# Performance work log

Hardware: AMD Instinct MI355X
Metric: run time of the kernel (lower is better)

## Reference

```python
import jax, jax.numpy as jnp
import numpy as np

N, D, M = 50000, 6, 32  # particles, state_dim, num_measurements
MD = 3                  # measurement dim (rho, alpha, epsilon)
_LOG2PI = jnp.log(2.0 * jnp.pi)


def h(x):
    # Radar measurement of a single state: uses position = x[:3]
    px, py, pz = x[0], x[1], x[2]
    rho = jnp.sqrt(px * px + py * py + pz * pz)
    return jnp.stack([rho, jnp.arctan2(py, px), jnp.arcsin(pz / rho)])


def setup_inputs() -> dict:
    key = jax.random.key(0)
    k1, k2, k3, k4 = jax.random.split(key, 4)
    scale = jnp.array([1000.0, 1000.0, 1000.0, 10.0, 10.0, 10.0], dtype=jnp.float32)
    offset = jnp.array([5000.0, 5000.0, 5000.0, 0.0, 0.0, 0.0], dtype=jnp.float32)
    means = jax.random.normal(k1, (N, D), dtype=jnp.float32) * scale + offset
    covs = jax.random.normal(k2, (N, D, D), dtype=jnp.float32)  # only used for zeros_like shape
    weights = jax.random.uniform(k3, (N,), dtype=jnp.float32)
    noise_std = jnp.array([1.0, jnp.deg2rad(0.5), jnp.deg2rad(0.5)], dtype=jnp.float32)
    measurements = jax.vmap(h)(means[:M]) + jax.random.normal(k4, (M, MD), dtype=jnp.float32) * noise_std
    measurements_mask = jnp.ones((M,), dtype=bool)
    R = jnp.diag(noise_std ** 2)  # measurement_system.covariance
    return {"means": means, "covs": covs, "weights": weights,
            "measurements": measurements, "measurements_mask": measurements_mask, "R": R}


def reference(means, covs, weights, measurements, measurements_mask, R):
    n, d = means.shape
    m = measurements.shape[0]
    md = measurements.shape[1]

    # Silverman-style bandwidth and localized empirical covariance (shared across particles)
    bandwidth = (4.0 / (n * (d + 2))) ** (2.0 / (d + 4))
    Xc = means - jnp.mean(means, axis=0)
    emp = (Xc.T @ Xc) / (n - 1)  # jnp.cov(means.T), ddof=1
    idx = jnp.arange(d)
    dist = jnp.abs(idx[:, None] - idx[None, :]).astype(means.dtype)
    rho_loc = jnp.exp(-dist ** 2 / (2.0 * 3.0 ** 2))  # L = 3.0
    P = bandwidth * (emp * rho_loc)  # [d, d] mixture covariance

    # Per-particle autodiff Jacobian of the measurement function (as in update_point)
    H = jax.vmap(jax.jacfwd(h))(means)                     # [N, md, d]
    S = jnp.einsum('nij,jk,nlk->nil', H, P, H) + R          # [N, md, md] innovation cov
    Sinv = jnp.linalg.inv(S)
    K = jnp.einsum('ij,nkj,nkl->nil', P, H, Sinv)           # [N, d, md] Kalman gain
    I = jnp.eye(d, dtype=means.dtype)
    KH = jnp.einsum('nik,nkj->nij', K, H)
    covs_post = jnp.einsum('nij,jk->nik', I - KH, P)        # [N, d, d]

    # Updated points per (measurement, particle)
    hx = jax.vmap(h)(means)                                 # [N, md]
    innov = hx[None, :, :] - measurements[:, None, :]       # [M, N, md] = h(x) - z
    pts = means[None, :, :] - jnp.einsum('ndk,mnk->mnd', K, innov)  # [M, N, d]

    # logpdf of measurement under N(h(updated point), S)
    h_post = jax.vmap(jax.vmap(h))(pts)                     # [M, N, md]
    diff = measurements[:, None, :] - h_post                # [M, N, md]
    L = jnp.linalg.cholesky(S)                              # [N, md, md]
    Lb = jnp.broadcast_to(L[None], (m, n, md, md))
    y = jax.scipy.linalg.solve_triangular(Lb, diff[..., None], lower=True)[..., 0]
    quad = jnp.sum(y * y, axis=-1)                          # [M, N]
    logdet = jnp.sum(jnp.log(jnp.diagonal(L, axis1=-2, axis2=-1)), axis=-1)  # [N]
    logw = -0.5 * quad - logdet[None, :] - 0.5 * md * _LOG2PI  # [M, N]

    # lax.cond on measurements_mask -> masked select of zeros / -inf
    mask = measurements_mask
    pts = jnp.where(mask[:, None, None], pts, jnp.zeros_like(means)[None])
    logw = jnp.where(mask[:, None], logw, -jnp.inf)
    covs_out = jnp.where(mask[:, None, None, None],
                         jnp.broadcast_to(covs_post[None], (m, n, d, d)),
                         jnp.zeros_like(covs)[None])
    return pts, logw, covs_out
```

## Files before the change

### kernel.cpp

```cpp
#include <hip/hip_runtime.h>
#include <math.h>


#define NDIM 6
#define MDIM 3
#define NB_STATS 128
#define MSPLIT 8
#define GROUP_M 4
#define CHUNK 128
typedef float f32x4 __attribute__((ext_vector_type(4)));

__device__ __forceinline__ bool mask_true(const int* m32, const unsigned char* m8, int m) {
    return (m32[m] != 0) || (m8[m] != 0);
}

__global__ __launch_bounds__(256) void stats_partial_kernel(const float* __restrict__ means,
                                                            int N, double* __restrict__ partials) {
    double sx[6];
    double sxx[21];
#pragma unroll
    for (int i = 0; i < 6; ++i) sx[i] = 0.0;
#pragma unroll
    for (int i = 0; i < 21; ++i) sxx[i] = 0.0;

    int stride = NB_STATS * 256;
    for (int n = blockIdx.x * 256 + threadIdx.x; n < N; n += stride) {
        const float2* mp = (const float2*)(means + (size_t)n * 6);
        float2 a = mp[0], b = mp[1], c = mp[2];
        double x[6] = {a.x, a.y, b.x, b.y, c.x, c.y};
        int p = 0;
#pragma unroll
        for (int i = 0; i < 6; ++i) {
            sx[i] += x[i];
#pragma unroll
            for (int j = i; j < 6; ++j) sxx[p++] += x[i] * x[j];
        }
    }
#pragma unroll
    for (int off = 32; off >= 1; off >>= 1) {
#pragma unroll
        for (int i = 0; i < 6; ++i) sx[i] += __shfl_down(sx[i], off);
#pragma unroll
        for (int i = 0; i < 21; ++i) sxx[i] += __shfl_down(sxx[i], off);
    }
    __shared__ double lds[4][27];
    int wave = threadIdx.x >> 6;
    if ((threadIdx.x & 63) == 0) {
#pragma unroll
        for (int i = 0; i < 6; ++i) lds[wave][i] = sx[i];
#pragma unroll
        for (int i = 0; i < 21; ++i) lds[wave][6 + i] = sxx[i];
    }
    __syncthreads();
    if (threadIdx.x < 27) {
        double v = lds[0][threadIdx.x] + lds[1][threadIdx.x] +
                   lds[2][threadIdx.x] + lds[3][threadIdx.x];
        partials[threadIdx.x * NB_STATS + blockIdx.x] = v;
    }
}

__global__ __launch_bounds__(256) void computeP_kernel(const double* __restrict__ partials,
                                                       int N, double* __restrict__ P64) {
    __shared__ double red[27][8];
    int tid = threadIdx.x;
    int s = tid >> 3, j = tid & 7;
    if (s < 27) {
        const double* src = partials + (size_t)s * NB_STATS + j * 16;
        double acc = 0.0;
#pragma unroll
        for (int k = 0; k < 16; ++k) acc += src[k];
        red[s][j] = acc;
    }
    __syncthreads();
    if (tid < 27) {
        double a = 0.0;
#pragma unroll
        for (int q = 0; q < 8; ++q) a += red[tid][q];
        red[tid][0] = a;
    }
    __syncthreads();
    if (tid == 0) {
        double mean[6];
#pragma unroll
        for (int i = 0; i < 6; ++i) mean[i] = red[i][0] / (double)N;
        double bandwidth = pow(4.0 / ((double)N * 8.0), 0.2);
        int p = 0;
        for (int i = 0; i < 6; ++i) {
            for (int jj = i; jj < 6; ++jj) {
                double emp = (red[6 + p][0] - (double)N * mean[i] * mean[jj]) / (double)(N - 1);
                double dd = (double)(jj - i);
                double val = bandwidth * emp * exp(-(dd * dd) / 18.0);
                P64[i * 6 + jj] = val;
                P64[jj * 6 + i] = val;
                ++p;
            }
        }
    }
}

struct PData {
    float hx0, hx1, hx2, logdet;
    float L00, L10, L11, L20, L21, L22;
    float Kf[6][3];
    float H[3][3];
};

__device__ __forceinline__ void particle_compute(const float* __restrict__ means,
                                                 const float* __restrict__ Rin,
                                                 const double* __restrict__ sP,
                                                 int n, float* __restrict__ x, PData& o) {
    const float2* mp = (const float2*)(means + (size_t)n * 6);
    float2 ma = mp[0], mb = mp[1], mc = mp[2];
    x[0] = ma.x; x[1] = ma.y; x[2] = mb.x; x[3] = mb.y; x[4] = mc.x; x[5] = mc.y;
    float px = ma.x, py = ma.y, pz = mb.x;
    float s2 = px * px + py * py;
    float r2 = s2 + pz * pz;
    float rho = sqrtf(r2);
    float s = sqrtf(s2);
    o.hx0 = rho;
    o.hx1 = atan2f(py, px);
    o.hx2 = asinf(pz / rho);
    o.H[0][0] = px / rho; o.H[0][1] = py / rho; o.H[0][2] = pz / rho;
    o.H[1][0] = -py / s2; o.H[1][1] = px / s2;  o.H[1][2] = 0.0f;
    float invr2s = 1.0f / (r2 * s);
    o.H[2][0] = -pz * px * invr2s; o.H[2][1] = -pz * py * invr2s; o.H[2][2] = s / r2;

    double T[3][3];
#pragma unroll
    for (int i = 0; i < 3; ++i)
#pragma unroll
        for (int k = 0; k < 3; ++k)
            T[i][k] = (double)o.H[i][0] * sP[0 * 6 + k] + (double)o.H[i][1] * sP[1 * 6 + k] +
                      (double)o.H[i][2] * sP[2 * 6 + k];
    double S[3][3];
#pragma unroll
    for (int i = 0; i < 3; ++i)
#pragma unroll
        for (int l = 0; l < 3; ++l)
            S[i][l] = T[i][0] * (double)o.H[l][0] + T[i][1] * (double)o.H[l][1] +
                      T[i][2] * (double)o.H[l][2] + (double)Rin[i * 3 + l];

    double L00 = sqrt(S[0][0]);
    double L10 = S[1][0] / L00;
    double L20 = S[2][0] / L00;
    double L11 = sqrt(S[1][1] - L10 * L10);
    double L21 = (S[2][1] - L20 * L10) / L11;
    double L22 = sqrt(S[2][2] - L20 * L20 - L21 * L21);
    o.L00 = (float)L00; o.L10 = (float)L10; o.L11 = (float)L11;
    o.L20 = (float)L20; o.L21 = (float)L21; o.L22 = (float)L22;
    o.logdet = logf((float)(L00 * L11 * L22));

    double a00 = S[0][0], a01 = S[0][1], a02 = S[0][2];
    double a11 = S[1][1], a12 = S[1][2], a22 = S[2][2];
    double c00 = a11 * a22 - a12 * a12;
    double c01 = a02 * a12 - a01 * a22;
    double c02 = a01 * a12 - a02 * a11;
    double c11 = a00 * a22 - a02 * a02;
    double c12 = a01 * a02 - a00 * a12;
    double c22 = a00 * a11 - a01 * a01;
    double invdet = 1.0 / (a00 * c00 + a01 * c01 + a02 * c02);
    double Si[3][3] = {{c00 * invdet, c01 * invdet, c02 * invdet},
                       {c01 * invdet, c11 * invdet, c12 * invdet},
                       {c02 * invdet, c12 * invdet, c22 * invdet}};

#pragma unroll
    for (int i = 0; i < 6; ++i) {
        double pht[3];
#pragma unroll
        for (int k = 0; k < 3; ++k)
            pht[k] = sP[i * 6 + 0] * (double)o.H[k][0] + sP[i * 6 + 1] * (double)o.H[k][1] +
                     sP[i * 6 + 2] * (double)o.H[k][2];
#pragma unroll
        for (int l = 0; l < 3; ++l)
            o.Kf[i][l] = (float)(pht[0] * Si[0][l] + pht[1] * Si[1][l] + pht[2] * Si[2][l]);
    }
}

__global__ __launch_bounds__(256) void fused_all_kernel(const float* __restrict__ means,
                                                        const float* __restrict__ meas,
                                                        const int* __restrict__ mask32,
                                                        const unsigned char* __restrict__ mask8,
                                                        const float* __restrict__ Rin,
                                                        const double* __restrict__ P64,
                                                        float* __restrict__ pts,
                                                        float* __restrict__ logw,
                                                        float* __restrict__ covs,
                                                        int N, int M, int CB, int TB,
                                                        int UBx) {
    __shared__ double sP[36];
    __shared__ float sPf[36];
    __shared__ float sbuf[CHUNK * 36];

    int tid = threadIdx.x;
    if (tid < 36) {
        double v = P64[tid];
        sP[tid] = v;
        sPf[tid] = (float)v;
    }
    __syncthreads();

    long long b = blockIdx.x;
    int cbef = (int)(b * CB / TB);
    int cnext = (int)((b + 1) * CB / TB);

    if (cnext > cbef) {
        int c = cbef / MSPLIT;
        int g = cbef - c * MSPLIT;
        int n0 = c * CHUNK;
        int count = N - n0;
        if (count > CHUNK) count = CHUNK;

        if (tid < count) {
            float x[6];
            PData o;
            particle_compute(means, Rin, sP, n0 + tid, x, o);
            float KH[6][3];
#pragma unroll
            for (int i = 0; i < 6; ++i)
#pragma unroll
                for (int j = 0; j < 3; ++j)
                    KH[i][j] = o.Kf[i][0] * o.H[0][j] + o.Kf[i][1] * o.H[1][j] +
                               o.Kf[i][2] * o.H[2][j];
            float* row = sbuf + tid * 36;
#pragma unroll
            for (int i = 0; i < 6; ++i)
#pragma unroll
                for (int j = 0; j < 6; ++j)
                    row[i * 6 + j] = sPf[i * 6 + j] - (KH[i][0] * sPf[0 * 6 + j] +
                                                       KH[i][1] * sPf[1 * 6 + j] +
                                                       KH[i][2] * sPf[2 * 6 + j]);
        }
        __syncthreads();

        int nf4 = count * 9;
        const f32x4* s4 = (const f32x4*)sbuf;
        f32x4 z = {0.f, 0.f, 0.f, 0.f};
        for (int m = g; m < M; m += MSPLIT) {
            bool mk = mask_true(mask32, mask8, m);
            f32x4* d4 = (f32x4*)covs + ((size_t)m * N + n0) * 9;
            if (mk) {
                for (int i = tid; i < nf4; i += 256) d4[i] = s4[i];
            } else {
                for (int i = tid; i < nf4; i += 256) d4[i] = z;
            }
        }
        return;
    }

    int u = (int)(b - cbef);
    int mg = u / UBx;
    int nb = u - mg * UBx;
    int n0 = nb * 256;
    int count = N - n0;
    if (count > 256) count = 256;

    float x[6];
    PData o;
    if (tid < count) particle_compute(means, Rin, sP, n0 + tid, x, o);

#pragma unroll
    for (int j = 0; j < GROUP_M; ++j) {
        int m = mg * GROUP_M + j;
        if (m >= M) break;
        bool mk = mask_true(mask32, mask8, m);
        __syncthreads();
        if (tid < count) {
            float pt[6];
            if (mk) {
                float z0 = meas[m * 3 + 0];
                float z1 = meas[m * 3 + 1];
                float z2v = meas[m * 3 + 2];
                float i0 = o.hx0 - z0, i1 = o.hx1 - z1, i2 = o.hx2 - z2v;
#pragma unroll
                for (int d = 0; d < 6; ++d)
                    pt[d] = x[d] - (o.Kf[d][0] * i0 + o.Kf[d][1] * i1 + o.Kf[d][2] * i2);
                float px = pt[0], py = pt[1], pz = pt[2];
                float r2 = px * px + py * py + pz * pz;
                float rho = sqrtf(r2);
                float d0 = z0 - rho;
                float d1 = z1 - atan2f(py, px);
                float d2 = z2v - asinf(pz / rho);
                float y0 = d0 / o.L00;
                float y1 = (d1 - o.L10 * y0) / o.L11;
                float y2 = (d2 - o.L20 * y0 - o.L21 * y1) / o.L22;
                float quad = y0 * y0 + y1 * y1 + y2 * y2;
                logw[(size_t)m * N + n0 + tid] = -0.5f * quad - o.logdet - 2.7568156f;
            } else {
#pragma unroll
                for (int d = 0; d < 6; ++d) pt[d] = 0.f;
                logw[(size_t)m * N + n0 + tid] = -INFINITY;
            }
#pragma unroll
            for (int d = 0; d < 6; ++d) sbuf[tid * 6 + d] = pt[d];
        }
        __syncthreads();
        int nf = count * 6;
        float* dst = pts + ((size_t)m * N + n0) * 6;
        const f32x4* s4 = (const f32x4*)sbuf;
        f32x4* d4 = (f32x4*)dst;
        int n4 = nf >> 2;
        for (int i = tid; i < n4; i += 256) d4[i] = s4[i];
        for (int i = (n4 << 2) + tid; i < nf; i += 256) dst[i] = sbuf[i];
    }
}

extern "C" void kernel_launch(void* const* d_in, const int* in_sizes, int n_in,
                              void* d_out, int out_size, void* d_ws, size_t ws_size,
                              hipStream_t stream) {
    const float* means = (const float*)d_in[0];
    const float* meas = (const float*)d_in[3];
    const int* mask32 = (const int*)d_in[4];
    const unsigned char* mask8 = (const unsigned char*)d_in[4];
    const float* Rin = (const float*)d_in[5];

    int N = in_sizes[0] / NDIM;
    int M = in_sizes[3] / MDIM;

    float* out = (float*)d_out;
    float* pts = out;
    float* logw = out + (size_t)M * N * 6;
    float* covs = out + (size_t)M * N * 7;

    double* partials = (double*)d_ws;
    double* P64 = partials + 27 * NB_STATS;

    int UBx = (N + 255) / 256;
    int MG = (M + GROUP_M - 1) / GROUP_M;
    int NC = (N + CHUNK - 1) / CHUNK;
    int CB = NC * MSPLIT;
    int UB = UBx * MG;
    int TB = CB + UB;

    stats_partial_kernel<<<NB_STATS, 256, 0, stream>>>(means, N, partials);
    computeP_kernel<<<1, 256, 0, stream>>>(partials, N, P64);
    fused_all_kernel<<<TB, 256, 0, stream>>>(means, meas, mask32, mask8, Rin,
                                             P64, pts, logw, covs, N, M, CB, TB, UBx);
}
```

Baseline: 65.16 us.

## Fold covariance finalization into main kernel and drop computeP launch

Result: no change. 64.02 us (-1.7%).

```diff
diff --git a/kernel.cpp b/kernel.cpp
--- a/kernel.cpp
+++ b/kernel.cpp
@@ -4,11 +4,15 @@
 
 #define NDIM 6
 #define MDIM 3
-#define NB_STATS 128
+#define NB_STATS 32
 #define MSPLIT 8
-#define GROUP_M 4
+#define GROUP_M 8
 #define CHUNK 128
 typedef float f32x4 __attribute__((ext_vector_type(4)));
+
+struct BW6 {
+    double w[6];
+};
 
 __device__ __forceinline__ bool mask_true(const int* m32, const unsigned char* m8, int m) {
     return (m32[m] != 0) || (m8[m] != 0);
@@ -56,45 +60,6 @@
         double v = lds[0][threadIdx.x] + lds[1][threadIdx.x] +
                    lds[2][threadIdx.x] + lds[3][threadIdx.x];
         partials[threadIdx.x * NB_STATS + blockIdx.x] = v;
-    }
-}
-
-__global__ __launch_bounds__(256) void computeP_kernel(const double* __restrict__ partials,
-                                                       int N, double* __restrict__ P64) {
-    __shared__ double red[27][8];
-    int tid = threadIdx.x;
-    int s = tid >> 3, j = tid & 7;
-    if (s < 27) {
-        const double* src = partials + (size_t)s * NB_STATS + j * 16;
-        double acc = 0.0;
-#pragma unroll
-        for (int k = 0; k < 16; ++k) acc += src[k];
-        red[s][j] = acc;
-    }
-    __syncthreads();
-    if (tid < 27) {
-        double a = 0.0;
-#pragma unroll
-        for (int q = 0; q < 8; ++q) a += red[tid][q];
-        red[tid][0] = a;
-    }
-    __syncthreads();
-    if (tid == 0) {
-        double mean[6];
-#pragma unroll
-        for (int i = 0; i < 6; ++i) mean[i] = red[i][0] / (double)N;
-        double bandwidth = pow(4.0 / ((double)N * 8.0), 0.2);
-        int p = 0;
-        for (int i = 0; i < 6; ++i) {
-            for (int jj = i; jj < 6; ++jj) {
-                double emp = (red[6 + p][0] - (double)N * mean[i] * mean[jj]) / (double)(N - 1);
-                double dd = (double)(jj - i);
-                double val = bandwidth * emp * exp(-(dd * dd) / 18.0);
-                P64[i * 6 + jj] = val;
-                P64[jj * 6 + i] = val;
-                ++p;
-            }
-        }
     }
 }
 
@@ -181,19 +146,36 @@
                                                         const int* __restrict__ mask32,
                                                         const unsigned char* __restrict__ mask8,
                                                         const float* __restrict__ Rin,
-                                                        const double* __restrict__ P64,
+                                                        const double* __restrict__ partials,
+                                                        BW6 bw,
                                                         float* __restrict__ pts,
                                                         float* __restrict__ logw,
                                                         float* __restrict__ covs,
                                                         int N, int M, int CB, int TB,
                                                         int UBx) {
+    __shared__ double sStats[27];
     __shared__ double sP[36];
     __shared__ float sPf[36];
     __shared__ float sbuf[CHUNK * 36];
 
     int tid = threadIdx.x;
+    if (tid < 27) {
+        const double* src = partials + (size_t)tid * NB_STATS;
+        double acc = 0.0;
+#pragma unroll
+        for (int k = 0; k < NB_STATS; ++k) acc += src[k];
+        sStats[tid] = acc;
+    }
+    __syncthreads();
     if (tid < 36) {
-        double v = P64[tid];
+        int ii = tid / 6, jj = tid - (tid / 6) * 6;
+        int a = ii < jj ? ii : jj;
+        int bb = ii < jj ? jj : ii;
+        int p = a * 6 - (a * (a - 1)) / 2 + (bb - a);
+        double mi = sStats[ii] / (double)N;
+        double mj = sStats[jj] / (double)N;
+        double emp = (sStats[6 + p] - (double)N * mi * mj) / (double)(N - 1);
+        double v = bw.w[bb - a] * emp;
         sP[tid] = v;
         sPf[tid] = (float)v;
     }
@@ -322,7 +304,11 @@
     float* covs = out + (size_t)M * N * 7;
 
     double* partials = (double*)d_ws;
-    double* P64 = partials + 27 * NB_STATS;
+
+    BW6 bw;
+    double bandwidth = pow(4.0 / ((double)N * 8.0), 0.2);
+    for (int d = 0; d < 6; ++d)
+        bw.w[d] = bandwidth * exp(-(double)(d * d) / 18.0);
 
     int UBx = (N + 255) / 256;
     int MG = (M + GROUP_M - 1) / GROUP_M;
@@ -332,7 +318,7 @@
     int TB = CB + UB;
 
     stats_partial_kernel<<<NB_STATS, 256, 0, stream>>>(means, N, partials);
-    computeP_kernel<<<1, 256, 0, stream>>>(partials, N, P64);
     fused_all_kernel<<<TB, 256, 0, stream>>>(means, meas, mask32, mask8, Rin,
-                                             P64, pts, logw, covs, N, M, CB, TB, UBx);
-}
+                                             partials, bw, pts, logw, covs,
+                                             N, M, CB, TB, UBx);
+}
```
